# Kernel tuning notes

Measured on AMD Instinct MI355X. Metric: run time of the kernel, lower is better.

Reference implementation:

```python
import jax, jax.numpy as jnp
import numpy as np

VOCAB, D, T, NC = 21128, 768, 4, 10
B, S = 64, 512


def setup_inputs() -> dict:
    key = jax.random.key(0)
    ks = jax.random.split(key, 12)
    inv = 1.0 / np.sqrt(D)
    return {
        "words": jax.random.randint(ks[0], (B, S), 0, VOCAB),
        "target": jax.random.randint(ks[1], (B, S), 0, T),
        "corpus": jax.random.randint(ks[2], (B,), 0, NC),
        "embed_table": jax.random.normal(ks[3], (VOCAB, D), jnp.float32) * 0.02,
        "shared_W": jax.random.uniform(ks[4], (D, T), jnp.float32, -inv, inv),
        "shared_b": jax.random.uniform(ks[5], (T,), jnp.float32, -inv, inv),
        "domain_A": jax.random.uniform(ks[6], (NC, D, T), jnp.float32, -inv, inv),
        "domain_b": jax.random.uniform(ks[7], (NC, T), jnp.float32, -inv, inv),
        "trans_m": jax.random.normal(ks[8], (T, T), jnp.float32) * 0.1,
        "start_scores": jax.random.normal(ks[9], (T,), jnp.float32) * 0.1,
        "end_scores": jax.random.normal(ks[10], (T,), jnp.float32) * 0.1,
    }


def reference(words, target, corpus, embed_table, shared_W, shared_b,
              domain_A, domain_b, trans_m, start_scores, end_scores):
    mask = words != 0                                    # (B,S) pad mask
    x = embed_table[words]                               # (B,S,D) embedding lookup
    # domain-gated projection: shared linear + per-corpus bmm
    out1 = jnp.einsum('bsd,dt->bst', x, shared_W) + shared_b
    A = domain_A[corpus]                                 # (B,D,T)
    bb = domain_b[corpus][:, None, :]                    # (B,1,T)
    out2 = jnp.einsum('bsd,bdt->bst', x, A) + bb
    logits = jax.nn.log_softmax(out1 + out2, axis=-1)    # (B,S,T)

    # --- CRF normalizer (forward algorithm, logsumexp scan over time) ---
    alpha0 = logits[:, 0] + start_scores[None, :]        # (B,T)

    def step(alpha, inp):
        logit_t, m_t = inp                               # (B,T), (B,)
        tmp = alpha[:, :, None] + logit_t[:, None, :] + trans_m[None, :, :]
        new = jax.nn.logsumexp(tmp, axis=1)              # (B,T)
        return jnp.where(m_t[:, None], new, alpha), None

    xs = (jnp.swapaxes(logits[:, 1:], 0, 1), jnp.swapaxes(mask[:, 1:], 0, 1))
    alpha, _ = jax.lax.scan(step, alpha0, xs)
    normalizer = jax.nn.logsumexp(alpha + end_scores[None, :], axis=1)  # (B,)

    # --- gold path score ---
    emit = jnp.take_along_axis(logits, target[..., None], axis=-1)[..., 0]  # (B,S)
    emit = jnp.where(mask, emit, 0.0)
    tr = trans_m[target[:, :-1], target[:, 1:]]          # (B,S-1)
    tr = jnp.where(mask[:, 1:], tr, 0.0)
    last_idx = jnp.maximum(jnp.sum(mask.astype(jnp.int32), axis=1) - 1, 0)
    bidx = jnp.arange(words.shape[0])
    gold = (emit.sum(1) + tr.sum(1)
            + start_scores[target[:, 0]]
            + end_scores[target[bidx, last_idx]])
    return normalizer - gold                             # (B,) NLL per sequence
```

## Files before the change

### kernel.cpp

```cpp
#include <hip/hip_runtime.h>

#define NB 64
#define NS 512
#define ND 768
#define NT 4
#define NC 10
#define NEG (-1e30f)

__global__ __launch_bounds__(256) void logits_kernel(
    const int* __restrict__ words, const int* __restrict__ corpus,
    const float* __restrict__ embed, const float* __restrict__ sW,
    const float* __restrict__ sb, const float* __restrict__ dA,
    const float* __restrict__ db, float* __restrict__ logits)
{
  __shared__ float4 Wl[ND];
  __shared__ float4 bl;

  const int tid = threadIdx.x;
  const int blk = blockIdx.x;
  const int b = blk >> 5;
  const int c = __builtin_amdgcn_readfirstlane(corpus[b]);

  const float4* sW4 = (const float4*)sW;
  const float4* dA4 = ((const float4*)dA) + (size_t)c * ND;
#pragma unroll
  for (int k = 0; k < 3; ++k) {
    const int d = tid + k * 256;
    const float4 a = sW4[d];
    const float4 e = dA4[d];
    Wl[d] = make_float4(a.x + e.x, a.y + e.y, a.z + e.z, a.w + e.w);
  }
  if (tid == 0) {
    const float4 a = *(const float4*)sb;
    const float4 e = ((const float4*)db)[c];
    bl = make_float4(a.x + e.x, a.y + e.y, a.z + e.z, a.w + e.w);
  }
  __syncthreads();

  const int lane = tid & 63;
  const int grp  = lane >> 4;
  const int q    = lane & 15;
  const int g    = blk * 16 + (tid >> 6) * 4 + grp;

  const int word = words[g];
  const float4* __restrict__ row4 = (const float4*)(embed + (size_t)word * ND);

  float a0 = 0.f, a1 = 0.f, a2 = 0.f, a3 = 0.f;
#pragma unroll
  for (int i = 0; i < 12; ++i) {
    const float4 xv = row4[i * 16 + q];
    const float4 w0 = Wl[i * 64 + q * 4 + 0];
    const float4 w1 = Wl[i * 64 + q * 4 + 1];
    const float4 w2 = Wl[i * 64 + q * 4 + 2];
    const float4 w3 = Wl[i * 64 + q * 4 + 3];
    a0 = fmaf(xv.x, w0.x, a0); a1 = fmaf(xv.x, w0.y, a1);
    a2 = fmaf(xv.x, w0.z, a2); a3 = fmaf(xv.x, w0.w, a3);
    a0 = fmaf(xv.y, w1.x, a0); a1 = fmaf(xv.y, w1.y, a1);
    a2 = fmaf(xv.y, w1.z, a2); a3 = fmaf(xv.y, w1.w, a3);
    a0 = fmaf(xv.z, w2.x, a0); a1 = fmaf(xv.z, w2.y, a1);
    a2 = fmaf(xv.z, w2.z, a2); a3 = fmaf(xv.z, w2.w, a3);
    a0 = fmaf(xv.w, w3.x, a0); a1 = fmaf(xv.w, w3.y, a1);
    a2 = fmaf(xv.w, w3.z, a2); a3 = fmaf(xv.w, w3.w, a3);
  }

#pragma unroll
  for (int off = 8; off; off >>= 1) {
    a0 += __shfl_xor(a0, off);
    a1 += __shfl_xor(a1, off);
    a2 += __shfl_xor(a2, off);
    a3 += __shfl_xor(a3, off);
  }

  if (q == 0) {
    a0 += bl.x; a1 += bl.y; a2 += bl.z; a3 += bl.w;
    const float m = fmaxf(fmaxf(a0, a1), fmaxf(a2, a3));
    const float sum = __expf(a0 - m) + __expf(a1 - m) +
                      __expf(a2 - m) + __expf(a3 - m);
    const float lse = m + __logf(sum);
    ((float4*)logits)[g] = make_float4(a0 - lse, a1 - lse, a2 - lse, a3 - lse);
  }
}

__global__ __launch_bounds__(256) void crf_kernel(
    const int* __restrict__ words, const int* __restrict__ target,
    const float* __restrict__ trans, const float* __restrict__ start_s,
    const float* __restrict__ end_s, const float* __restrict__ logits,
    float* __restrict__ out)
{
  const int tid = threadIdx.x;
  const int b = blockIdx.x;
  const int c = tid >> 2;
  const int a = tid & 3;

  __shared__ float bufA[64][16];
  __shared__ float bufB[32][16];
  __shared__ float wg[4];
  __shared__ int   wc[4];

  const float* lg = logits + (size_t)b * NS * NT;
  const int* wb = words + b * NS;
  const int* tb = target + b * NS;

  float gp = 0.f; int cp = 0;
#pragma unroll
  for (int q = 0; q < 2; ++q) {
    const int s = tid * 2 + q;
    if (wb[s] != 0) {
      const int t = tb[s];
      gp += lg[s * 4 + t];
      if (s > 0) gp += trans[tb[s - 1] * 4 + t];
      ++cp;
    }
  }
#pragma unroll
  for (int off = 32; off; off >>= 1) {
    gp += __shfl_xor(gp, off);
    cp += __shfl_xor(cp, off);
  }
  if ((tid & 63) == 0) { wg[tid >> 6] = gp; wc[tid >> 6] = cp; }

  float T[4][4];
#pragma unroll
  for (int i = 0; i < 4; ++i)
#pragma unroll
    for (int j = 0; j < 4; ++j) T[i][j] = trans[i * 4 + j];

  const int s_beg = 1 + c * 8;
  float4 lv[8]; int wm[8];
#pragma unroll
  for (int q = 0; q < 8; ++q) {
    const int s = s_beg + q;
    const bool in = s < NS;
    wm[q] = in ? wb[s] : 0;
    lv[q] = in ? *(const float4*)(lg + s * 4) : make_float4(0.f, 0.f, 0.f, 0.f);
  }

  float v0 = (a == 0) ? 0.f : NEG;
  float v1 = (a == 1) ? 0.f : NEG;
  float v2 = (a == 2) ? 0.f : NEG;
  float v3 = (a == 3) ? 0.f : NEG;
#pragma unroll
  for (int q = 0; q < 8; ++q) {
    if (wm[q] != 0) {
      const float4 l = lv[q];
      float t0, t1, t2, t3, m, sm;
      float n0, n1, n2, n3;
      t0 = v0 + T[0][0]; t1 = v1 + T[1][0]; t2 = v2 + T[2][0]; t3 = v3 + T[3][0];
      m = fmaxf(fmaxf(t0, t1), fmaxf(t2, t3));
      sm = __expf(t0 - m) + __expf(t1 - m) + __expf(t2 - m) + __expf(t3 - m);
      n0 = m + __logf(sm) + l.x;
      t0 = v0 + T[0][1]; t1 = v1 + T[1][1]; t2 = v2 + T[2][1]; t3 = v3 + T[3][1];
      m = fmaxf(fmaxf(t0, t1), fmaxf(t2, t3));
      sm = __expf(t0 - m) + __expf(t1 - m) + __expf(t2 - m) + __expf(t3 - m);
      n1 = m + __logf(sm) + l.y;
      t0 = v0 + T[0][2]; t1 = v1 + T[1][2]; t2 = v2 + T[2][2]; t3 = v3 + T[3][2];
      m = fmaxf(fmaxf(t0, t1), fmaxf(t2, t3));
      sm = __expf(t0 - m) + __expf(t1 - m) + __expf(t2 - m) + __expf(t3 - m);
      n2 = m + __logf(sm) + l.z;
      t0 = v0 + T[0][3]; t1 = v1 + T[1][3]; t2 = v2 + T[2][3]; t3 = v3 + T[3][3];
      m = fmaxf(fmaxf(t0, t1), fmaxf(t2, t3));
      sm = __expf(t0 - m) + __expf(t1 - m) + __expf(t2 - m) + __expf(t3 - m);
      n3 = m + __logf(sm) + l.w;
      v0 = n0; v1 = n1; v2 = n2; v3 = n3;
    }
  }
  bufA[c][a * 4 + 0] = v0;
  bufA[c][a * 4 + 1] = v1;
  bufA[c][a * 4 + 2] = v2;
  bufA[c][a * 4 + 3] = v3;

  float* src = &bufA[0][0];
  float* dst = &bufB[0][0];
  for (int n = 64; n > 1; n >>= 1) {
    const int entries = (n >> 1) * 16;
    __syncthreads();
    for (int e = tid; e < entries; e += 256) {
      const int p = e >> 4;
      const int aa = (e >> 2) & 3;
      const int jj = e & 3;
      const float* C1 = src + (2 * p) * 16;
      const float* C2 = src + (2 * p + 1) * 16;
      const float t0 = C1[aa * 4 + 0] + C2[0 * 4 + jj];
      const float t1 = C1[aa * 4 + 1] + C2[1 * 4 + jj];
      const float t2 = C1[aa * 4 + 2] + C2[2 * 4 + jj];
      const float t3 = C1[aa * 4 + 3] + C2[3 * 4 + jj];
      const float m = fmaxf(fmaxf(t0, t1), fmaxf(t2, t3));
      dst[p * 16 + aa * 4 + jj] =
          m + __logf(__expf(t0 - m) + __expf(t1 - m) + __expf(t2 - m) + __expf(t3 - m));
    }
    float* tmp = src; src = dst; dst = tmp;
  }
  __syncthreads();

  if (tid == 0) {
    const float* C = &bufA[0][0];
    const float4 l0 = *(const float4*)lg;
    const float a0 = l0.x + start_s[0];
    const float a1 = l0.y + start_s[1];
    const float a2 = l0.z + start_s[2];
    const float a3 = l0.w + start_s[3];
    float af[4];
#pragma unroll
    for (int j = 0; j < 4; ++j) {
      const float t0 = a0 + C[0 * 4 + j];
      const float t1 = a1 + C[1 * 4 + j];
      const float t2 = a2 + C[2 * 4 + j];
      const float t3 = a3 + C[3 * 4 + j];
      const float m = fmaxf(fmaxf(t0, t1), fmaxf(t2, t3));
      af[j] = m + __logf(__expf(t0 - m) + __expf(t1 - m) + __expf(t2 - m) + __expf(t3 - m));
    }
    const float z0 = af[0] + end_s[0], z1 = af[1] + end_s[1];
    const float z2 = af[2] + end_s[2], z3 = af[3] + end_s[3];
    const float mz = fmaxf(fmaxf(z0, z1), fmaxf(z2, z3));
    const float norm = mz + __logf(__expf(z0 - mz) + __expf(z1 - mz) +
                                   __expf(z2 - mz) + __expf(z3 - mz));

    float gold = wg[0] + wg[1] + wg[2] + wg[3];
    const int cnt = wc[0] + wc[1] + wc[2] + wc[3];
    const int last = (cnt - 1) > 0 ? (cnt - 1) : 0;
    gold += start_s[tb[0]] + end_s[tb[last]];
    out[b] = norm - gold;
  }
}

extern "C" void kernel_launch(void* const* d_in, const int* in_sizes, int n_in,
                              void* d_out, int out_size, void* d_ws, size_t ws_size,
                              hipStream_t stream) {
  const int*   words   = (const int*)d_in[0];
  const int*   target  = (const int*)d_in[1];
  const int*   corpus  = (const int*)d_in[2];
  const float* embed   = (const float*)d_in[3];
  const float* sW      = (const float*)d_in[4];
  const float* sb      = (const float*)d_in[5];
  const float* dA      = (const float*)d_in[6];
  const float* db      = (const float*)d_in[7];
  const float* trans   = (const float*)d_in[8];
  const float* start_s = (const float*)d_in[9];
  const float* end_s   = (const float*)d_in[10];
  float* out = (float*)d_out;
  float* logits = (float*)d_ws;

  logits_kernel<<<(NB * NS) / 16, 256, 0, stream>>>(words, corpus, embed, sW, sb, dA, db, logits);
  crf_kernel<<<NB, 256, 0, stream>>>(words, target, trans, start_s, end_s, logits, out);
}
```

Measured before the change: 30.51 us.

## Process two tokens per thread group in logits and widen CRF scan to 512 threads

```diff
diff --git a/kernel.cpp b/kernel.cpp
--- a/kernel.cpp
+++ b/kernel.cpp
@@ -6,6 +6,8 @@
 #define NT 4
 #define NC 10
 #define NEG (-1e30f)
+#define LOG2E 1.4426950408889634f
+#define LN2 0.6931471805599453f
 
 __global__ __launch_bounds__(256) void logits_kernel(
     const int* __restrict__ words, const int* __restrict__ corpus,
@@ -18,7 +20,7 @@
 
   const int tid = threadIdx.x;
   const int blk = blockIdx.x;
-  const int b = blk >> 5;
+  const int b = blk >> 4;
   const int c = __builtin_amdgcn_readfirstlane(corpus[b]);
 
   const float4* sW4 = (const float4*)sW;
@@ -40,48 +42,65 @@
   const int lane = tid & 63;
   const int grp  = lane >> 4;
   const int q    = lane & 15;
-  const int g    = blk * 16 + (tid >> 6) * 4 + grp;
-
-  const int word = words[g];
-  const float4* __restrict__ row4 = (const float4*)(embed + (size_t)word * ND);
+  const int gA   = blk * 32 + (tid >> 6) * 8 + grp * 2;
+  const int gB   = gA + 1;
+
+  const float4* __restrict__ rowA =
+      (const float4*)(embed + (size_t)words[gA] * ND);
+  const float4* __restrict__ rowB =
+      (const float4*)(embed + (size_t)words[gB] * ND);
 
   float a0 = 0.f, a1 = 0.f, a2 = 0.f, a3 = 0.f;
+  float b0 = 0.f, b1 = 0.f, b2 = 0.f, b3 = 0.f;
 #pragma unroll
   for (int i = 0; i < 12; ++i) {
-    const float4 xv = row4[i * 16 + q];
+    const float4 xa = rowA[i * 16 + q];
+    const float4 xb = rowB[i * 16 + q];
     const float4 w0 = Wl[i * 64 + q * 4 + 0];
     const float4 w1 = Wl[i * 64 + q * 4 + 1];
     const float4 w2 = Wl[i * 64 + q * 4 + 2];
     const float4 w3 = Wl[i * 64 + q * 4 + 3];
-    a0 = fmaf(xv.x, w0.x, a0); a1 = fmaf(xv.x, w0.y, a1);
-    a2 = fmaf(xv.x, w0.z, a2); a3 = fmaf(xv.x, w0.w, a3);
-    a0 = fmaf(xv.y, w1.x, a0); a1 = fmaf(xv.y, w1.y, a1);
-    a2 = fmaf(xv.y, w1.z, a2); a3 = fmaf(xv.y, w1.w, a3);
-    a0 = fmaf(xv.z, w2.x, a0); a1 = fmaf(xv.z, w2.y, a1);
-    a2 = fmaf(xv.z, w2.z, a2); a3 = fmaf(xv.z, w2.w, a3);
-    a0 = fmaf(xv.w, w3.x, a0); a1 = fmaf(xv.w, w3.y, a1);
-    a2 = fmaf(xv.w, w3.z, a2); a3 = fmaf(xv.w, w3.w, a3);
+    a0 = fmaf(xa.x, w0.x, a0); a1 = fmaf(xa.x, w0.y, a1);
+    a2 = fmaf(xa.x, w0.z, a2); a3 = fmaf(xa.x, w0.w, a3);
+    b0 = fmaf(xb.x, w0.x, b0); b1 = fmaf(xb.x, w0.y, b1);
+    b2 = fmaf(xb.x, w0.z, b2); b3 = fmaf(xb.x, w0.w, b3);
+    a0 = fmaf(xa.y, w1.x, a0); a1 = fmaf(xa.y, w1.y, a1);
+    a2 = fmaf(xa.y, w1.z, a2); a3 = fmaf(xa.y, w1.w, a3);
+    b0 = fmaf(xb.y, w1.x, b0); b1 = fmaf(xb.y, w1.y, b1);
+    b2 = fmaf(xb.y, w1.z, b2); b3 = fmaf(xb.y, w1.w, b3);
+    a0 = fmaf(xa.z, w2.x, a0); a1 = fmaf(xa.z, w2.y, a1);
+    a2 = fmaf(xa.z, w2.z, a2); a3 = fmaf(xa.z, w2.w, a3);
+    b0 = fmaf(xb.z, w2.x, b0); b1 = fmaf(xb.z, w2.y, b1);
+    b2 = fmaf(xb.z, w2.z, b2); b3 = fmaf(xb.z, w2.w, b3);
+    a0 = fmaf(xa.w, w3.x, a0); a1 = fmaf(xa.w, w3.y, a1);
+    a2 = fmaf(xa.w, w3.z, a2); a3 = fmaf(xa.w, w3.w, a3);
+    b0 = fmaf(xb.w, w3.x, b0); b1 = fmaf(xb.w, w3.y, b1);
+    b2 = fmaf(xb.w, w3.z, b2); b3 = fmaf(xb.w, w3.w, b3);
   }
 
 #pragma unroll
   for (int off = 8; off; off >>= 1) {
-    a0 += __shfl_xor(a0, off);
-    a1 += __shfl_xor(a1, off);
-    a2 += __shfl_xor(a2, off);
-    a3 += __shfl_xor(a3, off);
-  }
-
-  if (q == 0) {
-    a0 += bl.x; a1 += bl.y; a2 += bl.z; a3 += bl.w;
-    const float m = fmaxf(fmaxf(a0, a1), fmaxf(a2, a3));
-    const float sum = __expf(a0 - m) + __expf(a1 - m) +
-                      __expf(a2 - m) + __expf(a3 - m);
+    a0 += __shfl_xor(a0, off); a1 += __shfl_xor(a1, off);
+    a2 += __shfl_xor(a2, off); a3 += __shfl_xor(a3, off);
+    b0 += __shfl_xor(b0, off); b1 += __shfl_xor(b1, off);
+    b2 += __shfl_xor(b2, off); b3 += __shfl_xor(b3, off);
+  }
+
+  if (q < 2) {
+    float s0 = (q == 0) ? a0 : b0;
+    float s1 = (q == 0) ? a1 : b1;
+    float s2 = (q == 0) ? a2 : b2;
+    float s3 = (q == 0) ? a3 : b3;
+    s0 += bl.x; s1 += bl.y; s2 += bl.z; s3 += bl.w;
+    const float m = fmaxf(fmaxf(s0, s1), fmaxf(s2, s3));
+    const float sum = __expf(s0 - m) + __expf(s1 - m) +
+                      __expf(s2 - m) + __expf(s3 - m);
     const float lse = m + __logf(sum);
-    ((float4*)logits)[g] = make_float4(a0 - lse, a1 - lse, a2 - lse, a3 - lse);
+    ((float4*)logits)[gA + q] = make_float4(s0 - lse, s1 - lse, s2 - lse, s3 - lse);
   }
 }
 
-__global__ __launch_bounds__(256) void crf_kernel(
+__global__ __launch_bounds__(512) void crf_kernel(
     const int* __restrict__ words, const int* __restrict__ target,
     const float* __restrict__ trans, const float* __restrict__ start_s,
     const float* __restrict__ end_s, const float* __restrict__ logits,
@@ -92,75 +111,80 @@
   const int c = tid >> 2;
   const int a = tid & 3;
 
-  __shared__ float bufA[64][16];
-  __shared__ float bufB[32][16];
-  __shared__ float wg[4];
-  __shared__ int   wc[4];
+  __shared__ float bufA[128][16];
+  __shared__ float bufB[64][16];
+  __shared__ float wg[8];
+  __shared__ int   wc[8];
+  __shared__ float sT[16], sS[4], sE[4];
+
+  if (tid < 16) sT[tid] = trans[tid];
+  if (tid < 4)  { sS[tid] = start_s[tid]; sE[tid] = end_s[tid]; }
 
   const float* lg = logits + (size_t)b * NS * NT;
   const int* wb = words + b * NS;
   const int* tb = target + b * NS;
 
-  float gp = 0.f; int cp = 0;
-#pragma unroll
-  for (int q = 0; q < 2; ++q) {
-    const int s = tid * 2 + q;
-    if (wb[s] != 0) {
-      const int t = tb[s];
-      gp += lg[s * 4 + t];
-      if (s > 0) gp += trans[tb[s - 1] * 4 + t];
-      ++cp;
-    }
-  }
-#pragma unroll
-  for (int off = 32; off; off >>= 1) {
-    gp += __shfl_xor(gp, off);
-    cp += __shfl_xor(cp, off);
-  }
-  if ((tid & 63) == 0) { wg[tid >> 6] = gp; wc[tid >> 6] = cp; }
-
-  float T[4][4];
-#pragma unroll
-  for (int i = 0; i < 4; ++i)
-#pragma unroll
-    for (int j = 0; j < 4; ++j) T[i][j] = trans[i * 4 + j];
-
-  const int s_beg = 1 + c * 8;
-  float4 lv[8]; int wm[8];
-#pragma unroll
-  for (int q = 0; q < 8; ++q) {
+  const int s_beg = 1 + c * 4;
+  float4 lv[4]; int wm[4];
+#pragma unroll
+  for (int q = 0; q < 4; ++q) {
     const int s = s_beg + q;
     const bool in = s < NS;
     wm[q] = in ? wb[s] : 0;
     lv[q] = in ? *(const float4*)(lg + s * 4) : make_float4(0.f, 0.f, 0.f, 0.f);
   }
 
+  __syncthreads();
+
+  float T2[4][4];
+#pragma unroll
+  for (int i = 0; i < 4; ++i)
+#pragma unroll
+    for (int j = 0; j < 4; ++j) T2[i][j] = sT[i * 4 + j] * LOG2E;
+
+  float gp = 0.f; int cp = 0;
+  {
+    const int s = tid;
+    if (wb[s] != 0) {
+      const int t = tb[s];
+      gp += lg[s * 4 + t];
+      if (s > 0) gp += sT[tb[s - 1] * 4 + t];
+      ++cp;
+    }
+  }
+#pragma unroll
+  for (int off = 32; off; off >>= 1) {
+    gp += __shfl_xor(gp, off);
+    cp += __shfl_xor(cp, off);
+  }
+  if ((tid & 63) == 0) { wg[tid >> 6] = gp; wc[tid >> 6] = cp; }
+
   float v0 = (a == 0) ? 0.f : NEG;
   float v1 = (a == 1) ? 0.f : NEG;
   float v2 = (a == 2) ? 0.f : NEG;
   float v3 = (a == 3) ? 0.f : NEG;
 #pragma unroll
-  for (int q = 0; q < 8; ++q) {
+  for (int q = 0; q < 4; ++q) {
     if (wm[q] != 0) {
       const float4 l = lv[q];
       float t0, t1, t2, t3, m, sm;
       float n0, n1, n2, n3;
-      t0 = v0 + T[0][0]; t1 = v1 + T[1][0]; t2 = v2 + T[2][0]; t3 = v3 + T[3][0];
-      m = fmaxf(fmaxf(t0, t1), fmaxf(t2, t3));
-      sm = __expf(t0 - m) + __expf(t1 - m) + __expf(t2 - m) + __expf(t3 - m);
-      n0 = m + __logf(sm) + l.x;
-      t0 = v0 + T[0][1]; t1 = v1 + T[1][1]; t2 = v2 + T[2][1]; t3 = v3 + T[3][1];
-      m = fmaxf(fmaxf(t0, t1), fmaxf(t2, t3));
-      sm = __expf(t0 - m) + __expf(t1 - m) + __expf(t2 - m) + __expf(t3 - m);
-      n1 = m + __logf(sm) + l.y;
-      t0 = v0 + T[0][2]; t1 = v1 + T[1][2]; t2 = v2 + T[2][2]; t3 = v3 + T[3][2];
-      m = fmaxf(fmaxf(t0, t1), fmaxf(t2, t3));
-      sm = __expf(t0 - m) + __expf(t1 - m) + __expf(t2 - m) + __expf(t3 - m);
-      n2 = m + __logf(sm) + l.z;
-      t0 = v0 + T[0][3]; t1 = v1 + T[1][3]; t2 = v2 + T[2][3]; t3 = v3 + T[3][3];
-      m = fmaxf(fmaxf(t0, t1), fmaxf(t2, t3));
-      sm = __expf(t0 - m) + __expf(t1 - m) + __expf(t2 - m) + __expf(t3 - m);
-      n3 = m + __logf(sm) + l.w;
+      t0 = v0 + T2[0][0]; t1 = v1 + T2[1][0]; t2 = v2 + T2[2][0]; t3 = v3 + T2[3][0];
+      m = fmaxf(fmaxf(t0, t1), fmaxf(t2, t3));
+      sm = exp2f(t0 - m) + exp2f(t1 - m) + exp2f(t2 - m) + exp2f(t3 - m);
+      n0 = m + log2f(sm) + l.x * LOG2E;
+      t0 = v0 + T2[0][1]; t1 = v1 + T2[1][1]; t2 = v2 + T2[2][1]; t3 = v3 + T2[3][1];
+      m = fmaxf(fmaxf(t0, t1), fmaxf(t2, t3));
+      sm = exp2f(t0 - m) + exp2f(t1 - m) + exp2f(t2 - m) + exp2f(t3 - m);
+      n1 = m + log2f(sm) + l.y * LOG2E;
+      t0 = v0 + T2[0][2]; t1 = v1 + T2[1][2]; t2 = v2 + T2[2][2]; t3 = v3 + T2[3][2];
+      m = fmaxf(fmaxf(t0, t1), fmaxf(t2, t3));
+      sm = exp2f(t0 - m) + exp2f(t1 - m) + exp2f(t2 - m) + exp2f(t3 - m);
+      n2 = m + log2f(sm) + l.z * LOG2E;
+      t0 = v0 + T2[0][3]; t1 = v1 + T2[1][3]; t2 = v2 + T2[2][3]; t3 = v3 + T2[3][3];
+      m = fmaxf(fmaxf(t0, t1), fmaxf(t2, t3));
+      sm = exp2f(t0 - m) + exp2f(t1 - m) + exp2f(t2 - m) + exp2f(t3 - m);
+      n3 = m + log2f(sm) + l.w * LOG2E;
       v0 = n0; v1 = n1; v2 = n2; v3 = n3;
     }
   }
@@ -171,10 +195,10 @@
 
   float* src = &bufA[0][0];
   float* dst = &bufB[0][0];
-  for (int n = 64; n > 1; n >>= 1) {
+  for (int n = 128; n > 1; n >>= 1) {
     const int entries = (n >> 1) * 16;
     __syncthreads();
-    for (int e = tid; e < entries; e += 256) {
+    for (int e = tid; e < entries; e += 512) {
       const int p = e >> 4;
       const int aa = (e >> 2) & 3;
       const int jj = e & 3;
@@ -186,20 +210,21 @@
       const float t3 = C1[aa * 4 + 3] + C2[3 * 4 + jj];
       const float m = fmaxf(fmaxf(t0, t1), fmaxf(t2, t3));
       dst[p * 16 + aa * 4 + jj] =
-          m + __logf(__expf(t0 - m) + __expf(t1 - m) + __expf(t2 - m) + __expf(t3 - m));
+          m + log2f(exp2f(t0 - m) + exp2f(t1 - m) +
+                    exp2f(t2 - m) + exp2f(t3 - m));
     }
     float* tmp = src; src = dst; dst = tmp;
   }
   __syncthreads();
 
   if (tid == 0) {
-    const float* C = &bufA[0][0];
+    const float* C = src;
     const float4 l0 = *(const float4*)lg;
-    const float a0 = l0.x + start_s[0];
-    const float a1 = l0.y + start_s[1];
-    const float a2 = l0.z + start_s[2];
-    const float a3 = l0.w + start_s[3];
-    float af[4];
+    const float a0 = (l0.x + sS[0]) * LOG2E;
+    const float a1 = (l0.y + sS[1]) * LOG2E;
+    const float a2 = (l0.z + sS[2]) * LOG2E;
+    const float a3 = (l0.w + sS[3]) * LOG2E;
+    float z[4];
 #pragma unroll
     for (int j = 0; j < 4; ++j) {
       const float t0 = a0 + C[0 * 4 + j];
@@ -207,18 +232,17 @@
       const float t2 = a2 + C[2 * 4 + j];
       const float t3 = a3 + C[3 * 4 + j];
       const float m = fmaxf(fmaxf(t0, t1), fmaxf(t2, t3));
-      af[j] = m + __logf(__expf(t0 - m) + __expf(t1 - m) + __expf(t2 - m) + __expf(t3 - m));
-    }
-    const float z0 = af[0] + end_s[0], z1 = af[1] + end_s[1];
-    const float z2 = af[2] + end_s[2], z3 = af[3] + end_s[3];
-    const float mz = fmaxf(fmaxf(z0, z1), fmaxf(z2, z3));
-    const float norm = mz + __logf(__expf(z0 - mz) + __expf(z1 - mz) +
-                                   __expf(z2 - mz) + __expf(z3 - mz));
-
-    float gold = wg[0] + wg[1] + wg[2] + wg[3];
-    const int cnt = wc[0] + wc[1] + wc[2] + wc[3];
+      z[j] = m + log2f(exp2f(t0 - m) + exp2f(t1 - m) +
+                       exp2f(t2 - m) + exp2f(t3 - m)) + sE[j] * LOG2E;
+    }
+    const float mz = fmaxf(fmaxf(z[0], z[1]), fmaxf(z[2], z[3]));
+    const float norm = LN2 * (mz + log2f(exp2f(z[0] - mz) + exp2f(z[1] - mz) +
+                                         exp2f(z[2] - mz) + exp2f(z[3] - mz)));
+
+    float gold = wg[0] + wg[1] + wg[2] + wg[3] + wg[4] + wg[5] + wg[6] + wg[7];
+    const int cnt = wc[0] + wc[1] + wc[2] + wc[3] + wc[4] + wc[5] + wc[6] + wc[7];
     const int last = (cnt - 1) > 0 ? (cnt - 1) : 0;
-    gold += start_s[tb[0]] + end_s[tb[last]];
+    gold += sS[tb[0]] + sE[tb[last]];
     out[b] = norm - gold;
   }
 }
@@ -240,6 +264,6 @@
   float* out = (float*)d_out;
   float* logits = (float*)d_ws;
 
-  logits_kernel<<<(NB * NS) / 16, 256, 0, stream>>>(words, corpus, embed, sW, sb, dA, db, logits);
-  crf_kernel<<<NB, 256, 0, stream>>>(words, target, trans, start_s, end_s, logits, out);
+  logits_kernel<<<(NB * NS) / 32, 256, 0, stream>>>(words, corpus, embed, sW, sb, dA, db, logits);
+  crf_kernel<<<NB, 512, 0, stream>>>(words, target, trans, start_s, end_s, logits, out);
 }
```

Result: slower. 31.14 us (+2.1%).

## Fuse chunk CRF scan and gold-score partials into logits kernel

Applied to the files above, without the earlier changes.

```diff
diff --git a/kernel.cpp b/kernel.cpp
--- a/kernel.cpp
+++ b/kernel.cpp
@@ -7,20 +7,27 @@
 #define NC 10
 #define NEG (-1e30f)
 
-__global__ __launch_bounds__(256) void logits_kernel(
-    const int* __restrict__ words, const int* __restrict__ corpus,
-    const float* __restrict__ embed, const float* __restrict__ sW,
-    const float* __restrict__ sb, const float* __restrict__ dA,
-    const float* __restrict__ db, float* __restrict__ logits)
+__global__ __launch_bounds__(256) void logits_phaseA_kernel(
+    const int* __restrict__ words, const int* __restrict__ target,
+    const int* __restrict__ corpus, const float* __restrict__ embed,
+    const float* __restrict__ sW, const float* __restrict__ sb,
+    const float* __restrict__ dA, const float* __restrict__ db,
+    const float* __restrict__ trans,
+    float4* __restrict__ chunkM,
+    float*  __restrict__ partG,
+    int*    __restrict__ partC,
+    float4* __restrict__ l0ws)
 {
-  __shared__ float4 Wl[ND];
+  __shared__ float wt[NT][ND];
   __shared__ float4 bl;
+  __shared__ float4 lsm[16];
 
   const int tid = threadIdx.x;
   const int blk = blockIdx.x;
   const int b = blk >> 5;
+  const int j = blk & 31;
+
   const int c = __builtin_amdgcn_readfirstlane(corpus[b]);
-
   const float4* sW4 = (const float4*)sW;
   const float4* dA4 = ((const float4*)dA) + (size_t)c * ND;
 #pragma unroll
@@ -28,7 +35,10 @@
     const int d = tid + k * 256;
     const float4 a = sW4[d];
     const float4 e = dA4[d];
-    Wl[d] = make_float4(a.x + e.x, a.y + e.y, a.z + e.z, a.w + e.w);
+    wt[0][d] = a.x + e.x;
+    wt[1][d] = a.y + e.y;
+    wt[2][d] = a.z + e.z;
+    wt[3][d] = a.w + e.w;
   }
   if (tid == 0) {
     const float4 a = *(const float4*)sb;
@@ -37,38 +47,40 @@
   }
   __syncthreads();
 
-  const int lane = tid & 63;
-  const int grp  = lane >> 4;
-  const int q    = lane & 15;
-  const int g    = blk * 16 + (tid >> 6) * 4 + grp;
-
-  const int word = words[g];
-  const float4* __restrict__ row4 = (const float4*)(embed + (size_t)word * ND);
+  const int grp = tid >> 4;
+  const int q   = tid & 15;
+  const int g   = blk * 16 + grp;
+
+  const float4* __restrict__ row4 = (const float4*)(embed + (size_t)words[g] * ND);
+  const float4* __restrict__ Wt4 = (const float4*)&wt[0][0];
+
+  float4 x[12];
+#pragma unroll
+  for (int i = 0; i < 12; ++i) x[i] = row4[i * 16 + q];
 
   float a0 = 0.f, a1 = 0.f, a2 = 0.f, a3 = 0.f;
 #pragma unroll
   for (int i = 0; i < 12; ++i) {
-    const float4 xv = row4[i * 16 + q];
-    const float4 w0 = Wl[i * 64 + q * 4 + 0];
-    const float4 w1 = Wl[i * 64 + q * 4 + 1];
-    const float4 w2 = Wl[i * 64 + q * 4 + 2];
-    const float4 w3 = Wl[i * 64 + q * 4 + 3];
-    a0 = fmaf(xv.x, w0.x, a0); a1 = fmaf(xv.x, w0.y, a1);
-    a2 = fmaf(xv.x, w0.z, a2); a3 = fmaf(xv.x, w0.w, a3);
-    a0 = fmaf(xv.y, w1.x, a0); a1 = fmaf(xv.y, w1.y, a1);
-    a2 = fmaf(xv.y, w1.z, a2); a3 = fmaf(xv.y, w1.w, a3);
-    a0 = fmaf(xv.z, w2.x, a0); a1 = fmaf(xv.z, w2.y, a1);
-    a2 = fmaf(xv.z, w2.z, a2); a3 = fmaf(xv.z, w2.w, a3);
-    a0 = fmaf(xv.w, w3.x, a0); a1 = fmaf(xv.w, w3.y, a1);
-    a2 = fmaf(xv.w, w3.z, a2); a3 = fmaf(xv.w, w3.w, a3);
+    const float4 w0 = Wt4[0 * 192 + i * 16 + q];
+    const float4 w1 = Wt4[1 * 192 + i * 16 + q];
+    const float4 w2 = Wt4[2 * 192 + i * 16 + q];
+    const float4 w3 = Wt4[3 * 192 + i * 16 + q];
+    a0 = fmaf(x[i].x, w0.x, a0); a0 = fmaf(x[i].y, w0.y, a0);
+    a0 = fmaf(x[i].z, w0.z, a0); a0 = fmaf(x[i].w, w0.w, a0);
+    a1 = fmaf(x[i].x, w1.x, a1); a1 = fmaf(x[i].y, w1.y, a1);
+    a1 = fmaf(x[i].z, w1.z, a1); a1 = fmaf(x[i].w, w1.w, a1);
+    a2 = fmaf(x[i].x, w2.x, a2); a2 = fmaf(x[i].y, w2.y, a2);
+    a2 = fmaf(x[i].z, w2.z, a2); a2 = fmaf(x[i].w, w2.w, a2);
+    a3 = fmaf(x[i].x, w3.x, a3); a3 = fmaf(x[i].y, w3.y, a3);
+    a3 = fmaf(x[i].z, w3.z, a3); a3 = fmaf(x[i].w, w3.w, a3);
   }
 
 #pragma unroll
   for (int off = 8; off; off >>= 1) {
-    a0 += __shfl_xor(a0, off);
-    a1 += __shfl_xor(a1, off);
-    a2 += __shfl_xor(a2, off);
-    a3 += __shfl_xor(a3, off);
+    a0 += __shfl_xor(a0, off, 16);
+    a1 += __shfl_xor(a1, off, 16);
+    a2 += __shfl_xor(a2, off, 16);
+    a3 += __shfl_xor(a3, off, 16);
   }
 
   if (q == 0) {
@@ -77,97 +89,107 @@
     const float sum = __expf(a0 - m) + __expf(a1 - m) +
                       __expf(a2 - m) + __expf(a3 - m);
     const float lse = m + __logf(sum);
-    ((float4*)logits)[g] = make_float4(a0 - lse, a1 - lse, a2 - lse, a3 - lse);
+    lsm[grp] = make_float4(a0 - lse, a1 - lse, a2 - lse, a3 - lse);
+  }
+  __syncthreads();
+
+  if (tid < 16) {
+    const int s = j * 16 + tid;
+    float gp = 0.f; int cp = 0;
+    if (words[b * NS + s] != 0) {
+      const int t = target[b * NS + s];
+      const float4 lv = lsm[tid];
+      gp = (t == 0) ? lv.x : (t == 1) ? lv.y : (t == 2) ? lv.z : lv.w;
+      if (s > 0) gp += trans[target[b * NS + s - 1] * 4 + t];
+      cp = 1;
+    }
+#pragma unroll
+    for (int off = 8; off; off >>= 1) {
+      gp += __shfl_xor(gp, off, 16);
+      cp += __shfl_xor(cp, off, 16);
+    }
+    if (tid == 0) { partG[b * 32 + j] = gp; partC[b * 32 + j] = cp; }
+    if (tid == 0 && j == 0) l0ws[b] = lsm[0];
+  }
+
+  if (tid >= 64 && tid < 72) {
+    const int k = (tid - 64) >> 2;
+    const int a = tid & 3;
+    const int cg = j * 2 + k;
+    const int s_beg = (cg == 0) ? 1 : cg * 8;
+    const int s_end = cg * 8 + 8;
+
+    float T[4][4];
+#pragma unroll
+    for (int i = 0; i < 4; ++i)
+#pragma unroll
+      for (int t = 0; t < 4; ++t) T[i][t] = trans[i * 4 + t];
+
+    float v0 = (a == 0) ? 0.f : NEG;
+    float v1 = (a == 1) ? 0.f : NEG;
+    float v2 = (a == 2) ? 0.f : NEG;
+    float v3 = (a == 3) ? 0.f : NEG;
+    for (int s = s_beg; s < s_end; ++s) {
+      if (words[b * NS + s] != 0) {
+        const float4 l = lsm[s - j * 16];
+        float t0, t1, t2, t3, m, sm;
+        float n0, n1, n2, n3;
+        t0 = v0 + T[0][0]; t1 = v1 + T[1][0]; t2 = v2 + T[2][0]; t3 = v3 + T[3][0];
+        m = fmaxf(fmaxf(t0, t1), fmaxf(t2, t3));
+        sm = __expf(t0 - m) + __expf(t1 - m) + __expf(t2 - m) + __expf(t3 - m);
+        n0 = m + __logf(sm) + l.x;
+        t0 = v0 + T[0][1]; t1 = v1 + T[1][1]; t2 = v2 + T[2][1]; t3 = v3 + T[3][1];
+        m = fmaxf(fmaxf(t0, t1), fmaxf(t2, t3));
+        sm = __expf(t0 - m) + __expf(t1 - m) + __expf(t2 - m) + __expf(t3 - m);
+        n1 = m + __logf(sm) + l.y;
+        t0 = v0 + T[0][2]; t1 = v1 + T[1][2]; t2 = v2 + T[2][2]; t3 = v3 + T[3][2];
+        m = fmaxf(fmaxf(t0, t1), fmaxf(t2, t3));
+        sm = __expf(t0 - m) + __expf(t1 - m) + __expf(t2 - m) + __expf(t3 - m);
+        n2 = m + __logf(sm) + l.z;
+        t0 = v0 + T[0][3]; t1 = v1 + T[1][3]; t2 = v2 + T[2][3]; t3 = v3 + T[3][3];
+        m = fmaxf(fmaxf(t0, t1), fmaxf(t2, t3));
+        sm = __expf(t0 - m) + __expf(t1 - m) + __expf(t2 - m) + __expf(t3 - m);
+        n3 = m + __logf(sm) + l.w;
+        v0 = n0; v1 = n1; v2 = n2; v3 = n3;
+      }
+    }
+    chunkM[(size_t)(b * 64 + cg) * 4 + a] = make_float4(v0, v1, v2, v3);
   }
 }
 
-__global__ __launch_bounds__(256) void crf_kernel(
-    const int* __restrict__ words, const int* __restrict__ target,
-    const float* __restrict__ trans, const float* __restrict__ start_s,
-    const float* __restrict__ end_s, const float* __restrict__ logits,
-    float* __restrict__ out)
+__global__ __launch_bounds__(256) void crf_tree_kernel(
+    const int* __restrict__ target, const float* __restrict__ start_s,
+    const float* __restrict__ end_s, const float4* __restrict__ chunkM,
+    const float* __restrict__ partG, const int* __restrict__ partC,
+    const float4* __restrict__ l0ws, float* __restrict__ out)
 {
+  __shared__ float bufA[64][16];
+  __shared__ float bufB[32][16];
+  __shared__ float goldS;
+  __shared__ int   cntS;
+
   const int tid = threadIdx.x;
   const int b = blockIdx.x;
-  const int c = tid >> 2;
-  const int a = tid & 3;
-
-  __shared__ float bufA[64][16];
-  __shared__ float bufB[32][16];
-  __shared__ float wg[4];
-  __shared__ int   wc[4];
-
-  const float* lg = logits + (size_t)b * NS * NT;
-  const int* wb = words + b * NS;
-  const int* tb = target + b * NS;
-
-  float gp = 0.f; int cp = 0;
-#pragma unroll
-  for (int q = 0; q < 2; ++q) {
-    const int s = tid * 2 + q;
-    if (wb[s] != 0) {
-      const int t = tb[s];
-      gp += lg[s * 4 + t];
-      if (s > 0) gp += trans[tb[s - 1] * 4 + t];
-      ++cp;
-    }
-  }
-#pragma unroll
-  for (int off = 32; off; off >>= 1) {
-    gp += __shfl_xor(gp, off);
-    cp += __shfl_xor(cp, off);
-  }
-  if ((tid & 63) == 0) { wg[tid >> 6] = gp; wc[tid >> 6] = cp; }
-
-  float T[4][4];
-#pragma unroll
-  for (int i = 0; i < 4; ++i)
-#pragma unroll
-    for (int j = 0; j < 4; ++j) T[i][j] = trans[i * 4 + j];
-
-  const int s_beg = 1 + c * 8;
-  float4 lv[8]; int wm[8];
-#pragma unroll
-  for (int q = 0; q < 8; ++q) {
-    const int s = s_beg + q;
-    const bool in = s < NS;
-    wm[q] = in ? wb[s] : 0;
-    lv[q] = in ? *(const float4*)(lg + s * 4) : make_float4(0.f, 0.f, 0.f, 0.f);
-  }
-
-  float v0 = (a == 0) ? 0.f : NEG;
-  float v1 = (a == 1) ? 0.f : NEG;
-  float v2 = (a == 2) ? 0.f : NEG;
-  float v3 = (a == 3) ? 0.f : NEG;
-#pragma unroll
-  for (int q = 0; q < 8; ++q) {
-    if (wm[q] != 0) {
-      const float4 l = lv[q];
-      float t0, t1, t2, t3, m, sm;
-      float n0, n1, n2, n3;
-      t0 = v0 + T[0][0]; t1 = v1 + T[1][0]; t2 = v2 + T[2][0]; t3 = v3 + T[3][0];
-      m = fmaxf(fmaxf(t0, t1), fmaxf(t2, t3));
-      sm = __expf(t0 - m) + __expf(t1 - m) + __expf(t2 - m) + __expf(t3 - m);
-      n0 = m + __logf(sm) + l.x;
-      t0 = v0 + T[0][1]; t1 = v1 + T[1][1]; t2 = v2 + T[2][1]; t3 = v3 + T[3][1];
-      m = fmaxf(fmaxf(t0, t1), fmaxf(t2, t3));
-      sm = __expf(t0 - m) + __expf(t1 - m) + __expf(t2 - m) + __expf(t3 - m);
-      n1 = m + __logf(sm) + l.y;
-      t0 = v0 + T[0][2]; t1 = v1 + T[1][2]; t2 = v2 + T[2][2]; t3 = v3 + T[3][2];
-      m = fmaxf(fmaxf(t0, t1), fmaxf(t2, t3));
-      sm = __expf(t0 - m) + __expf(t1 - m) + __expf(t2 - m) + __expf(t3 - m);
-      n2 = m + __logf(sm) + l.z;
-      t0 = v0 + T[0][3]; t1 = v1 + T[1][3]; t2 = v2 + T[2][3]; t3 = v3 + T[3][3];
-      m = fmaxf(fmaxf(t0, t1), fmaxf(t2, t3));
-      sm = __expf(t0 - m) + __expf(t1 - m) + __expf(t2 - m) + __expf(t3 - m);
-      n3 = m + __logf(sm) + l.w;
-      v0 = n0; v1 = n1; v2 = n2; v3 = n3;
-    }
-  }
-  bufA[c][a * 4 + 0] = v0;
-  bufA[c][a * 4 + 1] = v1;
-  bufA[c][a * 4 + 2] = v2;
-  bufA[c][a * 4 + 3] = v3;
+
+  {
+    const int cc = tid >> 2, a = tid & 3;
+    const float4 v = chunkM[(size_t)(b * 64 + cc) * 4 + a];
+    bufA[cc][a * 4 + 0] = v.x;
+    bufA[cc][a * 4 + 1] = v.y;
+    bufA[cc][a * 4 + 2] = v.z;
+    bufA[cc][a * 4 + 3] = v.w;
+  }
+
+  if (tid < 32) {
+    float g = partG[b * 32 + tid];
+    int   cp = partC[b * 32 + tid];
+#pragma unroll
+    for (int off = 16; off; off >>= 1) {
+      g  += __shfl_xor(g, off, 32);
+      cp += __shfl_xor(cp, off, 32);
+    }
+    if (tid == 0) { goldS = g; cntS = cp; }
+  }
 
   float* src = &bufA[0][0];
   float* dst = &bufB[0][0];
@@ -186,7 +208,8 @@
       const float t3 = C1[aa * 4 + 3] + C2[3 * 4 + jj];
       const float m = fmaxf(fmaxf(t0, t1), fmaxf(t2, t3));
       dst[p * 16 + aa * 4 + jj] =
-          m + __logf(__expf(t0 - m) + __expf(t1 - m) + __expf(t2 - m) + __expf(t3 - m));
+          m + __logf(__expf(t0 - m) + __expf(t1 - m) +
+                     __expf(t2 - m) + __expf(t3 - m));
     }
     float* tmp = src; src = dst; dst = tmp;
   }
@@ -194,20 +217,21 @@
 
   if (tid == 0) {
     const float* C = &bufA[0][0];
-    const float4 l0 = *(const float4*)lg;
+    const float4 l0 = l0ws[b];
     const float a0 = l0.x + start_s[0];
     const float a1 = l0.y + start_s[1];
     const float a2 = l0.z + start_s[2];
     const float a3 = l0.w + start_s[3];
     float af[4];
 #pragma unroll
-    for (int j = 0; j < 4; ++j) {
-      const float t0 = a0 + C[0 * 4 + j];
-      const float t1 = a1 + C[1 * 4 + j];
-      const float t2 = a2 + C[2 * 4 + j];
-      const float t3 = a3 + C[3 * 4 + j];
+    for (int jj = 0; jj < 4; ++jj) {
+      const float t0 = a0 + C[0 * 4 + jj];
+      const float t1 = a1 + C[1 * 4 + jj];
+      const float t2 = a2 + C[2 * 4 + jj];
+      const float t3 = a3 + C[3 * 4 + jj];
       const float m = fmaxf(fmaxf(t0, t1), fmaxf(t2, t3));
-      af[j] = m + __logf(__expf(t0 - m) + __expf(t1 - m) + __expf(t2 - m) + __expf(t3 - m));
+      af[jj] = m + __logf(__expf(t0 - m) + __expf(t1 - m) +
+                          __expf(t2 - m) + __expf(t3 - m));
     }
     const float z0 = af[0] + end_s[0], z1 = af[1] + end_s[1];
     const float z2 = af[2] + end_s[2], z3 = af[3] + end_s[3];
@@ -215,10 +239,8 @@
     const float norm = mz + __logf(__expf(z0 - mz) + __expf(z1 - mz) +
                                    __expf(z2 - mz) + __expf(z3 - mz));
 
-    float gold = wg[0] + wg[1] + wg[2] + wg[3];
-    const int cnt = wc[0] + wc[1] + wc[2] + wc[3];
-    const int last = (cnt - 1) > 0 ? (cnt - 1) : 0;
-    gold += start_s[tb[0]] + end_s[tb[last]];
+    const int last = (cntS - 1) > 0 ? (cntS - 1) : 0;
+    const float gold = goldS + start_s[target[b * NS]] + end_s[target[b * NS + last]];
     out[b] = norm - gold;
   }
 }
@@ -238,8 +260,15 @@
   const float* start_s = (const float*)d_in[9];
   const float* end_s   = (const float*)d_in[10];
   float* out = (float*)d_out;
-  float* logits = (float*)d_ws;
-
-  logits_kernel<<<(NB * NS) / 16, 256, 0, stream>>>(words, corpus, embed, sW, sb, dA, db, logits);
-  crf_kernel<<<NB, 256, 0, stream>>>(words, target, trans, start_s, end_s, logits, out);
+
+  float4* chunkM = (float4*)d_ws;
+  float4* l0ws   = chunkM + (size_t)NB * 64 * 4;
+  float*  partG  = (float*)(l0ws + NB);
+  int*    partC  = (int*)(partG + NB * 32);
+
+  logits_phaseA_kernel<<<NB * 32, 256, 0, stream>>>(
+      words, target, corpus, embed, sW, sb, dA, db, trans,
+      chunkM, partG, partC, l0ws);
+  crf_tree_kernel<<<NB, 256, 0, stream>>>(
+      target, start_s, end_s, chunkM, partG, partC, l0ws, out);
 }
```

New measurement: 33.69 us. +10.4%, slower.
